# Kernel optimization log

Hardware: AMD Instinct MI355X
Metric: run time of the kernel (lower is better)

The kernel has to match this reference:

```python
import jax, jax.numpy as jnp
import numpy as np

N, E, G, H, D = 50000, 800000, 64, 2, 128  # nodes, edges, graphs, heads, out_channels
NEG_SLOPE_ATT = 0.2   # GATv2 default negative_slope
NEG_SLOPE_OUT = 0.01  # torch.nn.LeakyReLU default
BN_EPS = 1e-5


def setup_inputs() -> dict:
    key = jax.random.key(0)
    ks = jax.random.split(key, 12)
    x = jax.random.normal(ks[0], (N, 1), jnp.float32)
    edge_index = jax.random.randint(ks[1], (2, E), 0, N, dtype=jnp.int64)
    edge_attr = jax.random.normal(ks[2], (E,), jnp.float32)
    batch = jnp.sort(jax.random.randint(ks[3], (N,), 0, G, dtype=jnp.int64))
    # GATv2Conv params: lin_l/lin_r: Linear(1, H*D) with bias; lin_edge: Linear(1, H*D) no bias
    Wl = jax.random.normal(ks[4], (1, H * D), jnp.float32) * 0.5
    bl = jax.random.normal(ks[5], (H * D,), jnp.float32) * 0.1
    Wr = jax.random.normal(ks[6], (1, H * D), jnp.float32) * 0.5
    br = jax.random.normal(ks[7], (H * D,), jnp.float32) * 0.1
    We = jax.random.normal(ks[8], (1, H * D), jnp.float32) * 0.5
    att = jax.random.normal(ks[9], (H, D), jnp.float32) * 0.5
    bias = jax.random.normal(ks[10], (D,), jnp.float32) * 0.1
    gamma = jnp.ones((D,), jnp.float32)
    beta = jnp.zeros((D,), jnp.float32)
    return {"x": x, "edge_index": edge_index, "edge_attr": edge_attr, "batch": batch,
            "Wl": Wl, "bl": bl, "Wr": Wr, "br": br, "We": We, "att": att,
            "bias": bias, "gamma": gamma, "beta": beta}


def reference(x, edge_index, edge_attr, batch, Wl, bl, Wr, br, We, att, bias, gamma, beta):
    n = x.shape[0]
    src, dst = edge_index[0], edge_index[1]  # message flows src -> dst
    # node transforms: [N, H, D]
    xl = (x @ Wl + bl).reshape(n, H, D)  # lin_l (source side, also the message value)
    xr = (x @ Wr + br).reshape(n, H, D)  # lin_r (destination side)
    # edge feature embedding: [E, H, D]
    ee = (edge_attr[:, None] @ We).reshape(-1, H, D)
    # GATv2 scoring: leaky_relu(x_j + x_i + e), then dot with attention vector
    m = jax.nn.leaky_relu(xl[src] + xr[dst] + ee, NEG_SLOPE_ATT)  # [E, H, D]
    alpha = jnp.einsum('ehd,hd->eh', m, att)  # [E, H]
    # scatter-softmax over incoming edges per destination node
    amax = jax.ops.segment_max(alpha, dst, num_segments=n)  # [N, H]
    ea = jnp.exp(alpha - amax[dst])
    denom = jax.ops.segment_sum(ea, dst, num_segments=n)
    alpha = ea / (denom[dst] + 1e-16)
    # weighted scatter-add aggregation of x_j
    out = jax.ops.segment_sum(xl[src] * alpha[..., None], dst, num_segments=n)  # [N, H, D]
    out = out.mean(axis=1) + bias  # concat=False -> head average, then conv bias
    # BatchNorm1d in training mode (biased variance over nodes)
    mean = out.mean(axis=0)
    var = ((out - mean) ** 2).mean(axis=0)
    out = (out - mean) * jax.lax.rsqrt(var + BN_EPS) * gamma + beta
    out = jax.nn.leaky_relu(out, NEG_SLOPE_OUT)
    # graph-level scatter_add pooling
    return jax.ops.segment_sum(out, batch, num_segments=G)  # [G, D]
```

## Files before the change

kernel.cpp:

```cpp
#include <hip/hip_runtime.h>
#include <math.h>

#define NN 50000
#define NE 800000
#define NG 64

#define WS_C     0
#define WS_ACC   16
#define WS_BNSUM (WS_ACC + 4*NN)
#define WS_BNSQ  (WS_BNSUM + 128)
#define WS_MOM   WS_BNSUM
#define WS_HEAD  (WS_BNSQ + 128)
#define WS_STAGE (WS_HEAD + 4*NN)
#define WS_END   (WS_STAGE + 4*NE)
#define WS_NEED_BYTES ((size_t)WS_END * 4 + 256)

#define LEND 0xFFFFFFFFu

static_assert(((WS_STAGE * 4) % 16) == 0, "stage 16B alignment");
static_assert(NE % 8 == 0, "edge unroll");

#define STEP(wl_, wr_, we_, bb_, at_, xs_, xd_, ae_, acc_)                 \
  { float tt = fmaf(we_, ae_, bb_); tt = fmaf(wr_, xd_, tt);               \
    tt = fmaf(wl_, xs_, tt); acc_ = fmaf(fabsf(tt), at_, acc_); }

#define SMEM_WEIGHTS_DECL                                                  \
  __shared__ __align__(16) float sWl[256], sWr[256], sWe[256], sB[256], sAt[256];

#define SMEM_WEIGHTS_LOAD                                                  \
  for (int t_ = threadIdx.x; t_ < 256; t_ += blockDim.x) {                 \
    sWl[t_] = Wl[t_]; sWr[t_] = Wr[t_]; sWe[t_] = We[t_];                  \
    sB[t_] = bl[t_] + br[t_]; sAt[t_] = att[t_]; }                         \
  __syncthreads();

#define SCORES(xs_, xd_, ae_, accA, accB, out0, out1)                      \
  { float lin0 = fmaf(c0.x, xs_, fmaf(c0.y, xd_, fmaf(c0.z, ae_, c0.w))); \
    out0 = fmaf(0.4f, accA, 0.6f * lin0);                                  \
    float lin1 = fmaf(c1.x, xs_, fmaf(c1.y, xd_, fmaf(c1.z, ae_, c1.w))); \
    out1 = fmaf(0.4f, accB, 0.6f * lin1); }

#define STEP4(c, q0, q1, q2, q3)                                           \
  STEP(wl.c, wr.c, we.c, bb.c, at.c, xs0, xd0, ae0, q0)                    \
  STEP(wl.c, wr.c, we.c, bb.c, at.c, xs1, xd1, ae1, q1)                    \
  STEP(wl.c, wr.c, we.c, bb.c, at.c, xs2, xd2, ae2, q2)                    \
  STEP(wl.c, wr.c, we.c, bb.c, at.c, xs3, xd3, ae3, q3)

#define SCORE_CORE                                                         \
  int4 s4 = *(const int4*)&ei[base];                                       \
  int4 dd4 = *(const int4*)&ei[NE + base];                                 \
  float4 ae4 = *(const float4*)&eattr[base];                               \
  float xs0 = x[s4.x], xs1 = x[s4.y], xs2 = x[s4.z], xs3 = x[s4.w];        \
  float xd0 = x[dd4.x], xd1 = x[dd4.y], xd2 = x[dd4.z], xd3 = x[dd4.w];    \
  float ae0 = ae4.x, ae1 = ae4.y, ae2 = ae4.z, ae3 = ae4.w;

#define SCORE_LOOPS                                                        \
  float a00 = 0.f, a01 = 0.f, a02 = 0.f, a03 = 0.f;                        \
  float a10 = 0.f, a11 = 0.f, a12 = 0.f, a13 = 0.f;                        \
  _Pragma("unroll 2")                                                      \
  for (int j = 0; j < 128; j += 4) {                                       \
    float4 wl = *(const float4*)&sWl[j];                                   \
    float4 wr = *(const float4*)&sWr[j];                                   \
    float4 we = *(const float4*)&sWe[j];                                   \
    float4 bb = *(const float4*)&sB[j];                                    \
    float4 at = *(const float4*)&sAt[j];                                   \
    STEP4(x, a00, a01, a02, a03)                                           \
    STEP4(y, a00, a01, a02, a03)                                           \
    STEP4(z, a00, a01, a02, a03)                                           \
    STEP4(w, a00, a01, a02, a03)                                           \
  }                                                                        \
  _Pragma("unroll 2")                                                      \
  for (int j = 128; j < 256; j += 4) {                                     \
    float4 wl = *(const float4*)&sWl[j];                                   \
    float4 wr = *(const float4*)&sWr[j];                                   \
    float4 we = *(const float4*)&sWe[j];                                   \
    float4 bb = *(const float4*)&sB[j];                                    \
    float4 at = *(const float4*)&sAt[j];                                   \
    STEP4(x, a10, a11, a12, a13)                                           \
    STEP4(y, a10, a11, a12, a13)                                           \
    STEP4(z, a10, a11, a12, a13)                                           \
    STEP4(w, a10, a11, a12, a13)                                           \
  }                                                                        \
  float4 c0 = *(const float4*)&ws[WS_C];                                   \
  float4 c1 = *(const float4*)&ws[WS_C + 4];

#define STEP8(c, Q)                                                        \
  STEP(wl.c, wr.c, we.c, bb.c, at.c, xs0, xd0, ae0, Q##0)                  \
  STEP(wl.c, wr.c, we.c, bb.c, at.c, xs1, xd1, ae1, Q##1)                  \
  STEP(wl.c, wr.c, we.c, bb.c, at.c, xs2, xd2, ae2, Q##2)                  \
  STEP(wl.c, wr.c, we.c, bb.c, at.c, xs3, xd3, ae3, Q##3)                  \
  STEP(wl.c, wr.c, we.c, bb.c, at.c, xs4, xd4, ae4, Q##4)                  \
  STEP(wl.c, wr.c, we.c, bb.c, at.c, xs5, xd5, ae5, Q##5)                  \
  STEP(wl.c, wr.c, we.c, bb.c, at.c, xs6, xd6, ae6, Q##6)                  \
  STEP(wl.c, wr.c, we.c, bb.c, at.c, xs7, xd7, ae7, Q##7)

extern "C" __global__ __launch_bounds__(256)
void k0_init(float* __restrict__ ws,
             const float* __restrict__ att, const float* __restrict__ Wl,
             const float* __restrict__ Wr, const float* __restrict__ We,
             const float* __restrict__ bl, const float* __restrict__ br,
             float* __restrict__ out, int dense)
{
  int tid = blockIdx.x * 256 + threadIdx.x;
  int nt = gridDim.x * 256;
  if (dense) {
    unsigned* head = (unsigned*)(ws + WS_HEAD);
    for (int i = tid; i < 4 * NN; i += nt) head[i] = LEND;
    if (tid < 14) ws[WS_MOM + tid] = 0.f;
  } else {
    for (int i = tid; i < 4 * NN; i += nt) ws[WS_ACC + i] = 0.f;
    for (int i = tid; i < 256; i += nt) ws[WS_BNSUM + i] = 0.f;
  }
  for (int i = tid; i < NG * 128; i += nt) out[i] = 0.f;
  if (blockIdx.x == 0) {
    __shared__ float red[4][256];
    int t = threadIdx.x;
    float a = att[t];
    red[0][t] = a * Wl[t];
    red[1][t] = a * Wr[t];
    red[2][t] = a * We[t];
    red[3][t] = a * (bl[t] + br[t]);
    __syncthreads();
    if (t < 8) {
      int k = t >> 1, h = t & 1;
      float s = 0.f;
      for (int d = 0; d < 128; ++d) s += red[k][h * 128 + d];
      ws[WS_C + h * 4 + k] = s;
    }
  }
}

extern "C" __global__ __launch_bounds__(128, 1)
void ke_edge(const int* __restrict__ ei, const float* __restrict__ x,
             const float* __restrict__ eattr,
             const float* __restrict__ Wl, const float* __restrict__ Wr,
             const float* __restrict__ We, const float* __restrict__ bl,
             const float* __restrict__ br, const float* __restrict__ att,
             float* __restrict__ ws)
{
  SMEM_WEIGHTS_DECL
  SMEM_WEIGHTS_LOAD
  int base = (blockIdx.x * 128 + (int)threadIdx.x) * 8;
  if (base >= NE) return;
  int4 sa = *(const int4*)&ei[base];
  int4 sb = *(const int4*)&ei[base + 4];
  int4 da = *(const int4*)&ei[NE + base];
  int4 db = *(const int4*)&ei[NE + base + 4];
  float4 aea = *(const float4*)&eattr[base];
  float4 aeb = *(const float4*)&eattr[base + 4];
  float ae0 = aea.x, ae1 = aea.y, ae2 = aea.z, ae3 = aea.w;
  float ae4 = aeb.x, ae5 = aeb.y, ae6 = aeb.z, ae7 = aeb.w;
  unsigned* head = (unsigned*)(ws + WS_HEAD);
  unsigned pv0 = atomicExch(&head[4 * da.x + 0], (unsigned)(base + 0));
  unsigned pv1 = atomicExch(&head[4 * da.y + 1], (unsigned)(base + 1));
  unsigned pv2 = atomicExch(&head[4 * da.z + 2], (unsigned)(base + 2));
  unsigned pv3 = atomicExch(&head[4 * da.w + 3], (unsigned)(base + 3));
  unsigned pv4 = atomicExch(&head[4 * db.x + 0], (unsigned)(base + 4));
  unsigned pv5 = atomicExch(&head[4 * db.y + 1], (unsigned)(base + 5));
  unsigned pv6 = atomicExch(&head[4 * db.z + 2], (unsigned)(base + 6));
  unsigned pv7 = atomicExch(&head[4 * db.w + 3], (unsigned)(base + 7));
  float xs0 = x[sa.x], xs1 = x[sa.y], xs2 = x[sa.z], xs3 = x[sa.w];
  float xs4 = x[sb.x], xs5 = x[sb.y], xs6 = x[sb.z], xs7 = x[sb.w];
  float xd0 = x[da.x], xd1 = x[da.y], xd2 = x[da.z], xd3 = x[da.w];
  float xd4 = x[db.x], xd5 = x[db.y], xd6 = x[db.z], xd7 = x[db.w];
  float q0 = 0.f, q1 = 0.f, q2 = 0.f, q3 = 0.f;
  float q4 = 0.f, q5 = 0.f, q6 = 0.f, q7 = 0.f;
  float r0 = 0.f, r1 = 0.f, r2 = 0.f, r3 = 0.f;
  float r4 = 0.f, r5 = 0.f, r6 = 0.f, r7 = 0.f;
#pragma unroll 2
  for (int j = 0; j < 128; j += 4) {
    float4 wl = *(const float4*)&sWl[j];
    float4 wr = *(const float4*)&sWr[j];
    float4 we = *(const float4*)&sWe[j];
    float4 bb = *(const float4*)&sB[j];
    float4 at = *(const float4*)&sAt[j];
    STEP8(x, q) STEP8(y, q) STEP8(z, q) STEP8(w, q)
  }
#pragma unroll 2
  for (int j = 128; j < 256; j += 4) {
    float4 wl = *(const float4*)&sWl[j];
    float4 wr = *(const float4*)&sWr[j];
    float4 we = *(const float4*)&sWe[j];
    float4 bb = *(const float4*)&sB[j];
    float4 at = *(const float4*)&sAt[j];
    STEP8(x, r) STEP8(y, r) STEP8(z, r) STEP8(w, r)
  }
  float4 c0 = *(const float4*)&ws[WS_C];
  float4 c1 = *(const float4*)&ws[WS_C + 4];
  float4* stage = (float4*)(ws + WS_STAGE);
  float s0, s1;
#define EPI(i)                                                             \
  { SCORES(xs##i, xd##i, ae##i, q##i, r##i, s0, s1)                        \
    float e0 = __expf(s0), e1 = __expf(s1);                                \
    stage[base + i] = make_float4(e0, e1, xs##i, __uint_as_float(pv##i)); }
  EPI(0) EPI(1) EPI(2) EPI(3) EPI(4) EPI(5) EPI(6) EPI(7)
#undef EPI
}

extern "C" __global__ __launch_bounds__(256)
void kfm_gather(float* __restrict__ ws)
{
  const int t = threadIdx.x;
  int gid = blockIdx.x * 256 + t;
  int n = gid >> 2;
  int c = gid & 3;
  float f1 = 0.f, f2 = 0.f, f3 = 0.f, f4 = 0.f;
  float4 A = make_float4(0.f, 0.f, 0.f, 0.f);
  if (n < NN) {
    const unsigned* head = (const unsigned*)(ws + WS_HEAD);
    const float4* stage = (const float4*)(ws + WS_STAGE);
    unsigned p = head[gid];
    while (p != LEND) {
      float4 q = stage[p];
      p = __float_as_uint(q.w);
      A.x += q.x;
      A.y += q.y;
      A.z = fmaf(q.x, q.z, A.z);
      A.w = fmaf(q.y, q.z, A.w);
    }
  }
  A.x += __shfl_xor(A.x, 1); A.y += __shfl_xor(A.y, 1);
  A.z += __shfl_xor(A.z, 1); A.w += __shfl_xor(A.w, 1);
  A.x += __shfl_xor(A.x, 2); A.y += __shfl_xor(A.y, 2);
  A.z += __shfl_xor(A.z, 2); A.w += __shfl_xor(A.w, 2);
  if (n < NN && c == 0) {
    *(float4*)&ws[WS_ACC + 4 * n] = A;
    float r0 = 1.f / (A.x + 1e-16f);
    float r1 = 1.f / (A.y + 1e-16f);
    f1 = A.x * r0; f2 = A.z * r0; f3 = A.y * r1; f4 = A.w * r1;
  }
  float pm[14] = { f1, f2, f3, f4,
                   f1*f1, f1*f2, f1*f3, f1*f4,
                   f2*f2, f2*f3, f2*f4,
                   f3*f3, f3*f4, f4*f4 };
#pragma unroll
  for (int k = 0; k < 14; ++k) {
    float v = pm[k];
#pragma unroll
    for (int m = 32; m >= 1; m >>= 1) v += __shfl_xor(v, m);
    pm[k] = v;
  }
  __shared__ float smom[56];
  int wid = t >> 6, lane = t & 63;
  if (lane == 0) {
#pragma unroll
    for (int k = 0; k < 14; ++k) smom[wid * 14 + k] = pm[k];
  }
  __syncthreads();
  if (t < 14) {
    float s = smom[t] + smom[14 + t] + smom[28 + t] + smom[42 + t];
    if (s != 0.f) atomicAdd(&ws[WS_MOM + t], s);
  }
}

extern "C" __global__ __launch_bounds__(256)
void k4m_pool(const int* __restrict__ batch,
              const float* __restrict__ Wl, const float* __restrict__ bl,
              const float* __restrict__ bias, const float* __restrict__ gamma,
              const float* __restrict__ beta,
              float* __restrict__ ws, float* __restrict__ out)
{
  const int CHUNK = (NN + (int)gridDim.x - 1) / (int)gridDim.x;
  int n0 = blockIdx.x * CHUNK;
  if (n0 >= NN) return;
  int n1 = n0 + CHUNK; if (n1 > NN) n1 = NN;
  int t = threadIdx.x;
  int d = t & 127;
  int row = t >> 7;
  float S1 = ws[WS_MOM + 0], S2 = ws[WS_MOM + 1];
  float S3 = ws[WS_MOM + 2], S4 = ws[WS_MOM + 3];
  float M11 = ws[WS_MOM + 4], M12 = ws[WS_MOM + 5], M13 = ws[WS_MOM + 6];
  float M14 = ws[WS_MOM + 7], M22 = ws[WS_MOM + 8], M23 = ws[WS_MOM + 9];
  float M24 = ws[WS_MOM + 10], M33 = ws[WS_MOM + 11], M34 = ws[WS_MOM + 12];
  float M44 = ws[WS_MOM + 13];
  float g1 = 0.5f * bl[d], g2 = 0.5f * Wl[d];
  float g3 = 0.5f * bl[128 + d], g4 = 0.5f * Wl[128 + d];
  float g5 = bias[d];
  const float invN = 1.f / (float)NN;
  float dotS = g1 * S1 + g2 * S2 + g3 * S3 + g4 * S4;
  float mean = (dotS + (float)NN * g5) * invN;
  float sumsq = g1*g1*M11 + g2*g2*M22 + g3*g3*M33 + g4*g4*M44
              + 2.f*(g1*g2*M12 + g1*g3*M13 + g1*g4*M14
                   + g2*g3*M23 + g2*g4*M24 + g3*g4*M34)
              + 2.f*g5*dotS + (float)NN*g5*g5;
  float var = fmaf(sumsq, invN, -mean * mean);
  float scale = gamma[d] * rsqrtf(var + 1e-5f);
  float shift = fmaf(-mean, scale, beta[d]);
  __shared__ float pool[4][128];
  for (int i = t; i < 512; i += 256) ((float*)pool)[i] = 0.f;
  __syncthreads();
  int g0 = batch[n0];
  for (int n = n0 + row; n < n1; n += 2) {
    float4 a = *(const float4*)&ws[WS_ACC + 4 * n];
    float r0 = 1.f / (a.x + 1e-16f);
    float r1 = 1.f / (a.y + 1e-16f);
    float o = g1 * (a.x * r0) + g2 * (a.z * r0)
            + g3 * (a.y * r1) + g4 * (a.w * r1) + g5;
    float v = fmaf(o, scale, shift);
    v = v > 0.f ? v : 0.01f * v;
    int g = batch[n];
    int slot = g - g0;
    if (slot < 4) atomicAdd(&pool[slot][d], v);
    else atomicAdd(&out[g * 128 + d], v);
  }
  __syncthreads();
  for (int i = t; i < 512; i += 256) {
    int slot = i >> 7, dd = i & 127;
    int g = g0 + slot;
    float v = pool[slot][dd];
    if (g < NG && v != 0.f) atomicAdd(&out[g * 128 + dd], v);
  }
}

extern "C" __global__ __launch_bounds__(256)
void k12f(const int* __restrict__ ei, const float* __restrict__ x,
          const float* __restrict__ eattr,
          const float* __restrict__ Wl, const float* __restrict__ Wr,
          const float* __restrict__ We, const float* __restrict__ bl,
          const float* __restrict__ br, const float* __restrict__ att,
          float* __restrict__ ws)
{
  SMEM_WEIGHTS_DECL
  SMEM_WEIGHTS_LOAD
  int base = (blockIdx.x * 256 + threadIdx.x) * 4;
  if (base >= NE) return;
  SCORE_CORE
  SCORE_LOOPS
  float* acc = ws + WS_ACC;
  float s0, s1;
#define EPI2(xs_, xd_, ae_, accA, accB, dsti)                              \
  { SCORES(xs_, xd_, ae_, accA, accB, s0, s1)                              \
    float e0 = __expf(s0), e1 = __expf(s1);                                \
    float* a = &acc[4 * dsti];                                             \
    atomicAdd(a + 0, e0); atomicAdd(a + 1, e1);                            \
    atomicAdd(a + 2, e0 * xs_); atomicAdd(a + 3, e1 * xs_); }
  EPI2(xs0, xd0, ae0, a00, a10, dd4.x)
  EPI2(xs1, xd1, ae1, a01, a11, dd4.y)
  EPI2(xs2, xd2, ae2, a02, a12, dd4.z)
  EPI2(xs3, xd3, ae3, a03, a13, dd4.w)
#undef EPI2
}

__device__ __forceinline__ float node_out4(float4 a, float wl0, float wl1,
                                           float b0, float b1, float bs)
{
  float r0 = 1.f / (a.x + 1e-16f);
  float r1 = 1.f / (a.y + 1e-16f);
  return 0.5f * (fmaf(wl0, a.z * r0, b0 * (a.x * r0)) +
                 fmaf(wl1, a.w * r1, b1 * (a.y * r1))) + bs;
}

extern "C" __global__ __launch_bounds__(256)
void k3_stats(const float* __restrict__ Wl, const float* __restrict__ bl,
              const float* __restrict__ bias, float* __restrict__ ws)
{
  int d = threadIdx.x & 127;
  int row = threadIdx.x >> 7;
  float wl0 = Wl[d], wl1 = Wl[128 + d];
  float b0 = bl[d], b1 = bl[128 + d];
  float bs = bias[d];
  float sum = 0.f, sq = 0.f;
  for (int n = blockIdx.x * 2 + row; n < NN; n += gridDim.x * 2) {
    float4 a = *(const float4*)&ws[WS_ACC + 4 * n];
    float o = node_out4(a, wl0, wl1, b0, b1, bs);
    sum += o;
    sq = fmaf(o, o, sq);
  }
  __shared__ float l1[256], l2[256];
  l1[threadIdx.x] = sum; l2[threadIdx.x] = sq;
  __syncthreads();
  if (row == 0) {
    atomicAdd(&ws[WS_BNSUM + d], l1[d] + l1[128 + d]);
    atomicAdd(&ws[WS_BNSQ + d], l2[d] + l2[128 + d]);
  }
}

extern "C" __global__ __launch_bounds__(256)
void k4_pool(const int* __restrict__ batch,
             const float* __restrict__ Wl, const float* __restrict__ bl,
             const float* __restrict__ bias, const float* __restrict__ gamma,
             const float* __restrict__ beta,
             float* __restrict__ ws, float* __restrict__ out)
{
  const int CHUNK = (NN + (int)gridDim.x - 1) / (int)gridDim.x;
  int n0 = blockIdx.x * CHUNK;
  if (n0 >= NN) return;
  int n1 = n0 + CHUNK; if (n1 > NN) n1 = NN;
  int d = threadIdx.x & 127;
  int row = threadIdx.x >> 7;
  const float invN = 1.f / (float)NN;
  float mean = ws[WS_BNSUM + d] * invN;
  float var = fmaf(ws[WS_BNSQ + d], invN, -mean * mean);
  float scale = gamma[d] * rsqrtf(var + 1e-5f);
  float shift = fmaf(-mean, scale, beta[d]);
  float wl0 = Wl[d], wl1 = Wl[128 + d];
  float b0 = bl[d], b1 = bl[128 + d];
  float bs = bias[d];
  __shared__ float pool[4][128];
  for (int i = threadIdx.x; i < 512; i += 256) ((float*)pool)[i] = 0.f;
  __syncthreads();
  int g0 = batch[n0];
  for (int n = n0 + row; n < n1; n += 2) {
    float4 a = *(const float4*)&ws[WS_ACC + 4 * n];
    float o = node_out4(a, wl0, wl1, b0, b1, bs);
    float v = fmaf(o, scale, shift);
    v = v > 0.f ? v : 0.01f * v;
    int g = batch[n];
    int slot = g - g0;
    if (slot < 4) atomicAdd(&pool[slot][d], v);
    else atomicAdd(&out[g * 128 + d], v);
  }
  __syncthreads();
  for (int i = threadIdx.x; i < 512; i += 256) {
    int slot = i >> 7, dd = i & 127;
    int g = g0 + slot;
    float v = pool[slot][dd];
    if (g < NG && v != 0.f) atomicAdd(&out[g * 128 + dd], v);
  }
}

extern "C" void kernel_launch(void* const* d_in, const int* in_sizes, int n_in,
                              void* d_out, int out_size, void* d_ws, size_t ws_size,
                              hipStream_t stream) {
  const float* x     = (const float*)d_in[0];
  const int*   ei    = (const int*)d_in[1];
  const float* eattr = (const float*)d_in[2];
  const int*   batch = (const int*)d_in[3];
  const float* Wl    = (const float*)d_in[4];
  const float* bl    = (const float*)d_in[5];
  const float* Wr    = (const float*)d_in[6];
  const float* br    = (const float*)d_in[7];
  const float* We    = (const float*)d_in[8];
  const float* att   = (const float*)d_in[9];
  const float* bias  = (const float*)d_in[10];
  const float* gam   = (const float*)d_in[11];
  const float* bet   = (const float*)d_in[12];
  float* ws  = (float*)d_ws;
  float* out = (float*)d_out;

  const bool dense = (ws_size >= WS_NEED_BYTES);

  hipLaunchKernelGGL(k0_init, dim3(128), dim3(256), 0, stream,
                     ws, att, Wl, Wr, We, bl, br, out, dense ? 1 : 0);
  if (dense) {
    hipLaunchKernelGGL(ke_edge, dim3((NE / 8 + 127) / 128), dim3(128), 0, stream,
                       ei, x, eattr, Wl, Wr, We, bl, br, att, ws);
    hipLaunchKernelGGL(kfm_gather, dim3((4 * NN + 255) / 256), dim3(256), 0, stream, ws);
    hipLaunchKernelGGL(k4m_pool, dim3(256), dim3(256), 0, stream,
                       batch, Wl, bl, bias, gam, bet, ws, out);
  } else {
    hipLaunchKernelGGL(k12f, dim3((NE / 4 + 255) / 256), dim3(256), 0, stream,
                       ei, x, eattr, Wl, Wr, We, bl, br, att, ws);
    hipLaunchKernelGGL(k3_stats, dim3(256), dim3(256), 0, stream,
                       Wl, bl, bias, ws);
    hipLaunchKernelGGL(k4_pool, dim3(256), dim3(256), 0, stream,
                       batch, Wl, bl, bias, gam, bet, ws, out);
  }
}
```

Baseline: 206.2 us.

## Replace linked-list edge aggregation with bucketed counting sort and shared-memory reduction

Replaces the per-destination linked-list build (global atomicExch on head pointers) and its pointer-chasing gather with a counting sort. Edges are bucketed by destination>>8: each block keeps a per-bucket histogram, a single-block kernel prefix-scans the counts, a scatter kernel writes records into bucket order, and a gather kernel reduces each 256-node bucket through shared-memory atomics. This removes the serial dependent loads of the list walk and the head-array initialisation. In exchange it adds two extra launches, a single-block scan over 256x782 counts, and an extra full read and write pass over the 800k edge records.

Result: slower. 388.7 us (+88.5%).

```diff
diff --git a/kernel.cpp b/kernel.cpp
--- a/kernel.cpp
+++ b/kernel.cpp
@@ -4,21 +4,29 @@
 #define NN 50000
 #define NE 800000
 #define NG 64
+
+#define CB    1024
+#define NBLK  782
+#define NBUCK 196
+
+static_assert(NBLK * CB >= NE, "chunk cover");
+static_assert((NBUCK - 1) == (NN - 1) / 256, "bucket count");
 
 #define WS_C     0
 #define WS_ACC   16
 #define WS_BNSUM (WS_ACC + 4*NN)
 #define WS_BNSQ  (WS_BNSUM + 128)
 #define WS_MOM   WS_BNSUM
-#define WS_HEAD  (WS_BNSQ + 128)
-#define WS_STAGE (WS_HEAD + 4*NN)
-#define WS_END   (WS_STAGE + 4*NE)
+#define WS_EX    (WS_BNSQ + 128)
+#define WS_CNT   (WS_EX + 272)
+#define WS_REC0  (WS_CNT + 256*NBLK)
+#define WS_SORT  (WS_REC0 + 4*NE)
+#define WS_END   (WS_SORT + 4*NE)
 #define WS_NEED_BYTES ((size_t)WS_END * 4 + 256)
 
-#define LEND 0xFFFFFFFFu
-
-static_assert(((WS_STAGE * 4) % 16) == 0, "stage 16B alignment");
-static_assert(NE % 8 == 0, "edge unroll");
+static_assert(((WS_REC0 * 4) % 16) == 0, "rec0 16B alignment");
+static_assert(((WS_SORT * 4) % 16) == 0, "sort 16B alignment");
+static_assert(NE % 4 == 0, "edge unroll");
 
 #define STEP(wl_, wr_, we_, bb_, at_, xs_, xd_, ae_, acc_)                 \
   { float tt = fmaf(we_, ae_, bb_); tt = fmaf(wr_, xd_, tt);               \
@@ -28,7 +36,7 @@
   __shared__ __align__(16) float sWl[256], sWr[256], sWe[256], sB[256], sAt[256];
 
 #define SMEM_WEIGHTS_LOAD                                                  \
-  for (int t_ = threadIdx.x; t_ < 256; t_ += blockDim.x) {                 \
+  { int t_ = threadIdx.x;                                                  \
     sWl[t_] = Wl[t_]; sWr[t_] = Wr[t_]; sWe[t_] = We[t_];                  \
     sB[t_] = bl[t_] + br[t_]; sAt[t_] = att[t_]; }                         \
   __syncthreads();
@@ -83,16 +91,6 @@
   float4 c0 = *(const float4*)&ws[WS_C];                                   \
   float4 c1 = *(const float4*)&ws[WS_C + 4];
 
-#define STEP8(c, Q)                                                        \
-  STEP(wl.c, wr.c, we.c, bb.c, at.c, xs0, xd0, ae0, Q##0)                  \
-  STEP(wl.c, wr.c, we.c, bb.c, at.c, xs1, xd1, ae1, Q##1)                  \
-  STEP(wl.c, wr.c, we.c, bb.c, at.c, xs2, xd2, ae2, Q##2)                  \
-  STEP(wl.c, wr.c, we.c, bb.c, at.c, xs3, xd3, ae3, Q##3)                  \
-  STEP(wl.c, wr.c, we.c, bb.c, at.c, xs4, xd4, ae4, Q##4)                  \
-  STEP(wl.c, wr.c, we.c, bb.c, at.c, xs5, xd5, ae5, Q##5)                  \
-  STEP(wl.c, wr.c, we.c, bb.c, at.c, xs6, xd6, ae6, Q##6)                  \
-  STEP(wl.c, wr.c, we.c, bb.c, at.c, xs7, xd7, ae7, Q##7)
-
 extern "C" __global__ __launch_bounds__(256)
 void k0_init(float* __restrict__ ws,
              const float* __restrict__ att, const float* __restrict__ Wl,
@@ -103,8 +101,6 @@
   int tid = blockIdx.x * 256 + threadIdx.x;
   int nt = gridDim.x * 256;
   if (dense) {
-    unsigned* head = (unsigned*)(ws + WS_HEAD);
-    for (int i = tid; i < 4 * NN; i += nt) head[i] = LEND;
     if (tid < 14) ws[WS_MOM + tid] = 0.f;
   } else {
     for (int i = tid; i < 4 * NN; i += nt) ws[WS_ACC + i] = 0.f;
@@ -129,8 +125,8 @@
   }
 }
 
-extern "C" __global__ __launch_bounds__(128, 1)
-void ke_edge(const int* __restrict__ ei, const float* __restrict__ x,
+extern "C" __global__ __launch_bounds__(256, 2)
+void k_score(const int* __restrict__ ei, const float* __restrict__ x,
              const float* __restrict__ eattr,
              const float* __restrict__ Wl, const float* __restrict__ Wr,
              const float* __restrict__ We, const float* __restrict__ bl,
@@ -138,91 +134,104 @@
              float* __restrict__ ws)
 {
   SMEM_WEIGHTS_DECL
+  __shared__ unsigned cnt[256];
+  cnt[threadIdx.x] = 0u;
   SMEM_WEIGHTS_LOAD
-  int base = (blockIdx.x * 128 + (int)threadIdx.x) * 8;
-  if (base >= NE) return;
-  int4 sa = *(const int4*)&ei[base];
-  int4 sb = *(const int4*)&ei[base + 4];
-  int4 da = *(const int4*)&ei[NE + base];
-  int4 db = *(const int4*)&ei[NE + base + 4];
-  float4 aea = *(const float4*)&eattr[base];
-  float4 aeb = *(const float4*)&eattr[base + 4];
-  float ae0 = aea.x, ae1 = aea.y, ae2 = aea.z, ae3 = aea.w;
-  float ae4 = aeb.x, ae5 = aeb.y, ae6 = aeb.z, ae7 = aeb.w;
-  unsigned* head = (unsigned*)(ws + WS_HEAD);
-  unsigned pv0 = atomicExch(&head[4 * da.x + 0], (unsigned)(base + 0));
-  unsigned pv1 = atomicExch(&head[4 * da.y + 1], (unsigned)(base + 1));
-  unsigned pv2 = atomicExch(&head[4 * da.z + 2], (unsigned)(base + 2));
-  unsigned pv3 = atomicExch(&head[4 * da.w + 3], (unsigned)(base + 3));
-  unsigned pv4 = atomicExch(&head[4 * db.x + 0], (unsigned)(base + 4));
-  unsigned pv5 = atomicExch(&head[4 * db.y + 1], (unsigned)(base + 5));
-  unsigned pv6 = atomicExch(&head[4 * db.z + 2], (unsigned)(base + 6));
-  unsigned pv7 = atomicExch(&head[4 * db.w + 3], (unsigned)(base + 7));
-  float xs0 = x[sa.x], xs1 = x[sa.y], xs2 = x[sa.z], xs3 = x[sa.w];
-  float xs4 = x[sb.x], xs5 = x[sb.y], xs6 = x[sb.z], xs7 = x[sb.w];
-  float xd0 = x[da.x], xd1 = x[da.y], xd2 = x[da.z], xd3 = x[da.w];
-  float xd4 = x[db.x], xd5 = x[db.y], xd6 = x[db.z], xd7 = x[db.w];
-  float q0 = 0.f, q1 = 0.f, q2 = 0.f, q3 = 0.f;
-  float q4 = 0.f, q5 = 0.f, q6 = 0.f, q7 = 0.f;
-  float r0 = 0.f, r1 = 0.f, r2 = 0.f, r3 = 0.f;
-  float r4 = 0.f, r5 = 0.f, r6 = 0.f, r7 = 0.f;
-#pragma unroll 2
-  for (int j = 0; j < 128; j += 4) {
-    float4 wl = *(const float4*)&sWl[j];
-    float4 wr = *(const float4*)&sWr[j];
-    float4 we = *(const float4*)&sWe[j];
-    float4 bb = *(const float4*)&sB[j];
-    float4 at = *(const float4*)&sAt[j];
-    STEP8(x, q) STEP8(y, q) STEP8(z, q) STEP8(w, q)
-  }
-#pragma unroll 2
-  for (int j = 128; j < 256; j += 4) {
-    float4 wl = *(const float4*)&sWl[j];
-    float4 wr = *(const float4*)&sWr[j];
-    float4 we = *(const float4*)&sWe[j];
-    float4 bb = *(const float4*)&sB[j];
-    float4 at = *(const float4*)&sAt[j];
-    STEP8(x, r) STEP8(y, r) STEP8(z, r) STEP8(w, r)
-  }
-  float4 c0 = *(const float4*)&ws[WS_C];
-  float4 c1 = *(const float4*)&ws[WS_C + 4];
-  float4* stage = (float4*)(ws + WS_STAGE);
-  float s0, s1;
-#define EPI(i)                                                             \
-  { SCORES(xs##i, xd##i, ae##i, q##i, r##i, s0, s1)                        \
-    float e0 = __expf(s0), e1 = __expf(s1);                                \
-    stage[base + i] = make_float4(e0, e1, xs##i, __uint_as_float(pv##i)); }
-  EPI(0) EPI(1) EPI(2) EPI(3) EPI(4) EPI(5) EPI(6) EPI(7)
-#undef EPI
-}
-
-extern "C" __global__ __launch_bounds__(256)
-void kfm_gather(float* __restrict__ ws)
-{
+  int base = (blockIdx.x * 256 + threadIdx.x) * 4;
+  if (base < NE) {
+    SCORE_CORE
+    atomicAdd(&cnt[((unsigned)dd4.x) >> 8], 1u);
+    atomicAdd(&cnt[((unsigned)dd4.y) >> 8], 1u);
+    atomicAdd(&cnt[((unsigned)dd4.z) >> 8], 1u);
+    atomicAdd(&cnt[((unsigned)dd4.w) >> 8], 1u);
+    SCORE_LOOPS
+    float4* rec0 = (float4*)(ws + WS_REC0);
+    float s0, s1;
+    SCORES(xs0, xd0, ae0, a00, a10, s0, s1)
+    rec0[base + 0] = make_float4(__expf(s0), __expf(s1), xs0, __uint_as_float((unsigned)dd4.x));
+    SCORES(xs1, xd1, ae1, a01, a11, s0, s1)
+    rec0[base + 1] = make_float4(__expf(s0), __expf(s1), xs1, __uint_as_float((unsigned)dd4.y));
+    SCORES(xs2, xd2, ae2, a02, a12, s0, s1)
+    rec0[base + 2] = make_float4(__expf(s0), __expf(s1), xs2, __uint_as_float((unsigned)dd4.z));
+    SCORES(xs3, xd3, ae3, a03, a13, s0, s1)
+    rec0[base + 3] = make_float4(__expf(s0), __expf(s1), xs3, __uint_as_float((unsigned)dd4.w));
+  }
+  __syncthreads();
+  unsigned* counts = (unsigned*)(ws + WS_CNT);
+  counts[(size_t)threadIdx.x * NBLK + blockIdx.x] = cnt[threadIdx.x];
+}
+
+extern "C" __global__ __launch_bounds__(256)
+void k_scan(float* __restrict__ ws)
+{
+  int b = threadIdx.x;
+  unsigned* counts = (unsigned*)(ws + WS_CNT);
+  unsigned* row = counts + (size_t)b * NBLK;
+  unsigned run = 0;
+#pragma unroll 4
+  for (int k = 0; k < NBLK; ++k) { unsigned t = row[k]; row[k] = run; run += t; }
+  __shared__ unsigned sc[256];
+  sc[b] = run;
+  __syncthreads();
+  for (int o = 1; o < 256; o <<= 1) {
+    unsigned v = (b >= o) ? sc[b - o] : 0u;
+    __syncthreads();
+    sc[b] += v;
+    __syncthreads();
+  }
+  unsigned* ex = (unsigned*)(ws + WS_EX);
+  ex[b] = sc[b] - run;
+  if (b == 255) ex[256] = sc[b];
+}
+
+extern "C" __global__ __launch_bounds__(256)
+void k_scatter(float* __restrict__ ws)
+{
+  __shared__ unsigned soff[256];
+  int blk = blockIdx.x, tid = threadIdx.x;
+  const unsigned* counts = (const unsigned*)(ws + WS_CNT);
+  const unsigned* ex = (const unsigned*)(ws + WS_EX);
+  soff[tid] = ex[tid] + counts[(size_t)tid * NBLK + blk];
+  __syncthreads();
+  const float4* rec0 = (const float4*)(ws + WS_REC0);
+  float4* srt = (float4*)(ws + WS_SORT);
+  int e0i = blk * CB + tid;
+#pragma unroll
+  for (int i = 0; i < 4; ++i) {
+    int e = e0i + i * 256;
+    if (e < NE) {
+      float4 r = rec0[e];
+      unsigned d = __float_as_uint(r.w);
+      unsigned p = atomicAdd(&soff[d >> 8], 1u);
+      srt[p] = r;
+    }
+  }
+}
+
+extern "C" __global__ __launch_bounds__(256)
+void k_gather(float* __restrict__ ws)
+{
+  int b = blockIdx.x;
   const int t = threadIdx.x;
-  int gid = blockIdx.x * 256 + t;
-  int n = gid >> 2;
-  int c = gid & 3;
+  __shared__ float acc[1024];
+  acc[t] = 0.f; acc[256 + t] = 0.f; acc[512 + t] = 0.f; acc[768 + t] = 0.f;
+  __syncthreads();
+  const unsigned* ex = (const unsigned*)(ws + WS_EX);
+  int lo = (int)ex[b], hi = (int)ex[b + 1];
+  const float4* srt = (const float4*)(ws + WS_SORT);
+  for (int i = lo + t; i < hi; i += 256) {
+    float4 r = srt[i];
+    int l4 = (int)(__float_as_uint(r.w) & 255u) * 4;
+    atomicAdd(&acc[l4 + 0], r.x);
+    atomicAdd(&acc[l4 + 1], r.y);
+    atomicAdd(&acc[l4 + 2], r.x * r.z);
+    atomicAdd(&acc[l4 + 3], r.y * r.z);
+  }
+  __syncthreads();
+  int n = (b << 8) + t;
   float f1 = 0.f, f2 = 0.f, f3 = 0.f, f4 = 0.f;
-  float4 A = make_float4(0.f, 0.f, 0.f, 0.f);
   if (n < NN) {
-    const unsigned* head = (const unsigned*)(ws + WS_HEAD);
-    const float4* stage = (const float4*)(ws + WS_STAGE);
-    unsigned p = head[gid];
-    while (p != LEND) {
-      float4 q = stage[p];
-      p = __float_as_uint(q.w);
-      A.x += q.x;
-      A.y += q.y;
-      A.z = fmaf(q.x, q.z, A.z);
-      A.w = fmaf(q.y, q.z, A.w);
-    }
-  }
-  A.x += __shfl_xor(A.x, 1); A.y += __shfl_xor(A.y, 1);
-  A.z += __shfl_xor(A.z, 1); A.w += __shfl_xor(A.w, 1);
-  A.x += __shfl_xor(A.x, 2); A.y += __shfl_xor(A.y, 2);
-  A.z += __shfl_xor(A.z, 2); A.w += __shfl_xor(A.w, 2);
-  if (n < NN && c == 0) {
+    float4 A = make_float4(acc[t * 4], acc[t * 4 + 1], acc[t * 4 + 2], acc[t * 4 + 3]);
     *(float4*)&ws[WS_ACC + 4 * n] = A;
     float r0 = 1.f / (A.x + 1e-16f);
     float r1 = 1.f / (A.y + 1e-16f);
@@ -248,7 +257,7 @@
   __syncthreads();
   if (t < 14) {
     float s = smom[t] + smom[14 + t] + smom[28 + t] + smom[42 + t];
-    if (s != 0.f) atomicAdd(&ws[WS_MOM + t], s);
+    atomicAdd(&ws[WS_MOM + t], s);
   }
 }
 
@@ -439,12 +448,14 @@
 
   const bool dense = (ws_size >= WS_NEED_BYTES);
 
-  hipLaunchKernelGGL(k0_init, dim3(128), dim3(256), 0, stream,
+  hipLaunchKernelGGL(k0_init, dim3(32), dim3(256), 0, stream,
                      ws, att, Wl, Wr, We, bl, br, out, dense ? 1 : 0);
   if (dense) {
-    hipLaunchKernelGGL(ke_edge, dim3((NE / 8 + 127) / 128), dim3(128), 0, stream,
+    hipLaunchKernelGGL(k_score, dim3(NBLK), dim3(256), 0, stream,
                        ei, x, eattr, Wl, Wr, We, bl, br, att, ws);
-    hipLaunchKernelGGL(kfm_gather, dim3((4 * NN + 255) / 256), dim3(256), 0, stream, ws);
+    hipLaunchKernelGGL(k_scan, dim3(1), dim3(256), 0, stream, ws);
+    hipLaunchKernelGGL(k_scatter, dim3(NBLK), dim3(256), 0, stream, ws);
+    hipLaunchKernelGGL(k_gather, dim3(NBUCK), dim3(256), 0, stream, ws);
     hipLaunchKernelGGL(k4m_pool, dim3(256), dim3(256), 0, stream,
                        batch, Wl, bl, bias, gam, bet, ws, out);
   } else {
```
